# Optimization experiments

Hardware: AMD Instinct MI355X
Metric: run time of the kernel (lower is better)

Reference implementation:

```python
import jax, jax.numpy as jnp
import numpy as np

B, N, P, E = 4096, 1024, 32, 16  # batch, generator dim, n_params, expand_ratio


def setup_inputs() -> dict:
    key = jax.random.key(0)
    k1, k2, k3 = jax.random.split(key, 3)
    x = jax.random.normal(k1, (B, N), dtype=jnp.float32)
    # params ~ stdv*rand - stdv as in the module (stdv=0.01)
    params = 0.01 * jax.random.uniform(k2, (P, E), dtype=jnp.float32) - 0.01
    transformations = jax.random.normal(k3, (P, N, N), dtype=jnp.float32)
    return {"x": x, "params": params, "transformations": transformations}


def reference(x, params, transformations):
    # Fused version of the per-dim loop in ExpandFilterFunctionNew2:
    # filter_e = (params[:, e] @ transformations.flatten(1)).reshape(N, N)
    P_, N_, _ = transformations.shape
    E_ = params.shape[-1]
    filters = jnp.einsum('pe,pq->eq', params, transformations.reshape(P_, -1))
    filters = filters.reshape(E_, N_, N_)              # [E, N, N]
    # output[b, i, e] = sum_j filter[e, i, j] * x[b, j]
    out = jnp.einsum('eij,bj->bie', filters, x)        # [B, N, E]
    # Swish activation (add_linear=False path)
    return out * jax.nn.sigmoid(out)
```

## Files before the change

kernel.cpp:

```cpp
#include <hip/hip_runtime.h>
#include <hip/hip_bf16.h>
#include <stdint.h>

#define BB 4096
#define NN 1024
#define PP 32
#define EE 16
#define NC (NN*EE)

#define BM 256
#define BN 256
#define BK 64
#define NT (NN/BK)

typedef __bf16 bf16x8 __attribute__((ext_vector_type(8)));
typedef float  f32x4  __attribute__((ext_vector_type(4)));

__device__ __forceinline__ void gl2lds16(const void* g, void* l) {
  __builtin_amdgcn_global_load_lds(
      (const __attribute__((address_space(1))) void*)g,
      (__attribute__((address_space(3))) void*)l,
      16, 0, 0);
}

__global__ __launch_bounds__(256) void cvt_x_kernel(
    const float* __restrict__ x, __hip_bfloat16* __restrict__ xb) {
  size_t i4 = (size_t)blockIdx.x * 256 + threadIdx.x;
  float4 v = ((const float4*)x)[i4];
  union { __hip_bfloat16 h[4]; ushort4 u; } pk;
  pk.h[0] = __float2bfloat16(v.x);
  pk.h[1] = __float2bfloat16(v.y);
  pk.h[2] = __float2bfloat16(v.z);
  pk.h[3] = __float2bfloat16(v.w);
  *(ushort4*)(xb + i4 * 4) = pk.u;
}

__global__ __launch_bounds__(256) void make_filters(
    const float* __restrict__ params,
    const float* __restrict__ T,
    __hip_bfloat16* __restrict__ Gt) {
  const int tid = threadIdx.x;
  const int i = blockIdx.x;
  const int j = tid * 4;
  const float4* Tv = (const float4*)T;
  const size_t qv = ((size_t)i * NN + j) >> 2;
  const size_t SLABQ = (size_t)NN * NN / 4;

  float acc[EE][4];
#pragma unroll
  for (int e = 0; e < EE; ++e) {
    acc[e][0] = 0.f; acc[e][1] = 0.f; acc[e][2] = 0.f; acc[e][3] = 0.f;
  }

#pragma unroll 1
  for (int p = 0; p < PP; p += 4) {
    float4 t0 = Tv[(size_t)(p + 0) * SLABQ + qv];
    float4 t1 = Tv[(size_t)(p + 1) * SLABQ + qv];
    float4 t2 = Tv[(size_t)(p + 2) * SLABQ + qv];
    float4 t3 = Tv[(size_t)(p + 3) * SLABQ + qv];
#pragma unroll
    for (int e = 0; e < EE; ++e) {
      float w0 = params[(p + 0) * EE + e];
      float w1 = params[(p + 1) * EE + e];
      float w2 = params[(p + 2) * EE + e];
      float w3 = params[(p + 3) * EE + e];
      acc[e][0] += w0 * t0.x; acc[e][1] += w0 * t0.y;
      acc[e][2] += w0 * t0.z; acc[e][3] += w0 * t0.w;
      acc[e][0] += w1 * t1.x; acc[e][1] += w1 * t1.y;
      acc[e][2] += w1 * t1.z; acc[e][3] += w1 * t1.w;
      acc[e][0] += w2 * t2.x; acc[e][1] += w2 * t2.y;
      acc[e][2] += w2 * t2.z; acc[e][3] += w2 * t2.w;
      acc[e][0] += w3 * t3.x; acc[e][1] += w3 * t3.y;
      acc[e][2] += w3 * t3.z; acc[e][3] += w3 * t3.w;
    }
  }

#pragma unroll
  for (int e = 0; e < EE; ++e) {
    union { __hip_bfloat16 h[4]; ushort4 u; } pk;
    pk.h[0] = __float2bfloat16(acc[e][0]);
    pk.h[1] = __float2bfloat16(acc[e][1]);
    pk.h[2] = __float2bfloat16(acc[e][2]);
    pk.h[3] = __float2bfloat16(acc[e][3]);
    *(ushort4*)&Gt[((size_t)i * EE + e) * NN + j] = pk.u;
  }
}

__global__ __launch_bounds__(512, 2) void gemm_swish(
    const __hip_bfloat16* __restrict__ A,
    const __hip_bfloat16* __restrict__ Bt,
    float* __restrict__ C) {
  __shared__ __hip_bfloat16 lds[2][2][BM * BK];

  const int tid  = threadIdx.x;
  const int wv   = tid >> 6;
  const int lane = tid & 63;
  const int bn   = blockIdx.x;
  const int bm   = blockIdx.y;

  const int srow = wv * 8 + (lane >> 3);
  const int scol = ((lane & 7) ^ (lane >> 3)) * 8;
  const __hip_bfloat16* aSrc = A  + ((size_t)bm * BM + srow) * NN + scol;
  const __hip_bfloat16* bSrc = Bt + ((size_t)bn * BN + srow) * NN + scol;

  const int wm   = (wv >> 2) * 128;
  const int wn   = (wv & 3) * 64;
  const int lrow = lane & 15;
  const int g    = lane >> 4;
  const int xr   = lane & 7;

  f32x4 acc[8][4] = {};

  auto stage = [&](int n_) {
    const int s_  = n_ & 1;
    const int k0_ = n_ * BK;
    char* la = (char*)&lds[s_][0][0] + wv * 1024;
    char* lb = (char*)&lds[s_][1][0] + wv * 1024;
#pragma unroll
    for (int i = 0; i < 4; ++i) {
      gl2lds16(aSrc + (size_t)i * 64 * NN + k0_, la + i * 8192);
      gl2lds16(bSrc + (size_t)i * 64 * NN + k0_, lb + i * 8192);
    }
  };

  stage(0);
  __syncthreads();

  for (int n = 0; n < NT; ++n) {
    if (n + 1 < NT) stage(n + 1);

    const int s = n & 1;
#pragma unroll
    for (int kk = 0; kk < 2; ++kk) {
      bf16x8 af[8], bf[4];
#pragma unroll
      for (int mt = 0; mt < 8; ++mt) {
        const int row = wm + mt * 16 + lrow;
        const int ch  = (kk * 4 + g) ^ xr;
        af[mt] = *(const bf16x8*)&lds[s][0][row * 64 + ch * 8];
      }
#pragma unroll
      for (int nt = 0; nt < 4; ++nt) {
        const int row = wn + nt * 16 + lrow;
        const int ch  = (kk * 4 + g) ^ xr;
        bf[nt] = *(const bf16x8*)&lds[s][1][row * 64 + ch * 8];
      }
#pragma unroll
      for (int mt = 0; mt < 8; ++mt)
#pragma unroll
        for (int nt = 0; nt < 4; ++nt)
          acc[mt][nt] = __builtin_amdgcn_mfma_f32_16x16x32_bf16(
              af[mt], bf[nt], acc[mt][nt], 0, 0, 0);
    }

    __syncthreads();
  }

  const size_t row0 = (size_t)bm * BM + wm + (lane >> 4) * 4;
  const size_t col0 = (size_t)bn * BN + wn + (lane & 15);
#pragma unroll
  for (int mt = 0; mt < 8; ++mt) {
#pragma unroll
    for (int nt = 0; nt < 4; ++nt) {
      const size_t col = col0 + nt * 16;
#pragma unroll
      for (int r = 0; r < 4; ++r) {
        float o = acc[mt][nt][r];
        float s = o * __builtin_amdgcn_rcpf(1.0f + __expf(-o));
        C[(row0 + mt * 16 + r) * NC + col] = s;
      }
    }
  }
}

extern "C" void kernel_launch(void* const* d_in, const int* in_sizes, int n_in,
                              void* d_out, int out_size, void* d_ws, size_t ws_size,
                              hipStream_t stream) {
  const float* x      = (const float*)d_in[0];
  const float* params = (const float*)d_in[1];
  const float* T      = (const float*)d_in[2];
  float* out = (float*)d_out;

  __hip_bfloat16* Gt = (__hip_bfloat16*)d_ws;
  __hip_bfloat16* xb = (__hip_bfloat16*)((char*)d_ws + (size_t)NC * NN * 2);

  cvt_x_kernel<<<(BB * NN / 4) / 256, 256, 0, stream>>>(x, xb);
  make_filters<<<NN, 256, 0, stream>>>(params, T, Gt);
  gemm_swish<<<dim3(NC / BN, BB / BM), 512, 0, stream>>>(xb, Gt, out);
}
```

Baseline: 471.5 us.

## Split GEMM prefetch across k-halves, add barrier and MFMA priority boost

```diff
diff --git a/kernel.cpp b/kernel.cpp
--- a/kernel.cpp
+++ b/kernel.cpp
@@ -53,25 +53,19 @@
   }
 
 #pragma unroll 1
-  for (int p = 0; p < PP; p += 4) {
-    float4 t0 = Tv[(size_t)(p + 0) * SLABQ + qv];
-    float4 t1 = Tv[(size_t)(p + 1) * SLABQ + qv];
-    float4 t2 = Tv[(size_t)(p + 2) * SLABQ + qv];
-    float4 t3 = Tv[(size_t)(p + 3) * SLABQ + qv];
+  for (int p0 = 0; p0 < PP; p0 += 8) {
+    float4 t[8];
 #pragma unroll
-    for (int e = 0; e < EE; ++e) {
-      float w0 = params[(p + 0) * EE + e];
-      float w1 = params[(p + 1) * EE + e];
-      float w2 = params[(p + 2) * EE + e];
-      float w3 = params[(p + 3) * EE + e];
-      acc[e][0] += w0 * t0.x; acc[e][1] += w0 * t0.y;
-      acc[e][2] += w0 * t0.z; acc[e][3] += w0 * t0.w;
-      acc[e][0] += w1 * t1.x; acc[e][1] += w1 * t1.y;
-      acc[e][2] += w1 * t1.z; acc[e][3] += w1 * t1.w;
-      acc[e][0] += w2 * t2.x; acc[e][1] += w2 * t2.y;
-      acc[e][2] += w2 * t2.z; acc[e][3] += w2 * t2.w;
-      acc[e][0] += w3 * t3.x; acc[e][1] += w3 * t3.y;
-      acc[e][2] += w3 * t3.z; acc[e][3] += w3 * t3.w;
+    for (int u = 0; u < 8; ++u)
+      t[u] = Tv[(size_t)(p0 + u) * SLABQ + qv];
+#pragma unroll
+    for (int u = 0; u < 8; ++u) {
+#pragma unroll
+      for (int e = 0; e < EE; ++e) {
+        float w = params[(p0 + u) * EE + e];
+        acc[e][0] += w * t[u].x; acc[e][1] += w * t[u].y;
+        acc[e][2] += w * t[u].z; acc[e][3] += w * t[u].w;
+      }
     }
   }
 
@@ -111,46 +105,44 @@
 
   f32x4 acc[8][4] = {};
 
-  auto stage = [&](int n_) {
+  auto stage_half = [&](int n_, int h_) {
     const int s_  = n_ & 1;
     const int k0_ = n_ * BK;
-    char* la = (char*)&lds[s_][0][0] + wv * 1024;
-    char* lb = (char*)&lds[s_][1][0] + wv * 1024;
+    const __hip_bfloat16* src = h_ ? bSrc : aSrc;
+    char* dst = (char*)&lds[s_][h_][0] + wv * 1024;
 #pragma unroll
-    for (int i = 0; i < 4; ++i) {
-      gl2lds16(aSrc + (size_t)i * 64 * NN + k0_, la + i * 8192);
-      gl2lds16(bSrc + (size_t)i * 64 * NN + k0_, lb + i * 8192);
-    }
+    for (int i = 0; i < 4; ++i)
+      gl2lds16(src + (size_t)i * 64 * NN + k0_, dst + i * 8192);
   };
 
-  stage(0);
+  stage_half(0, 0);
+  stage_half(0, 1);
   __syncthreads();
 
   for (int n = 0; n < NT; ++n) {
-    if (n + 1 < NT) stage(n + 1);
-
     const int s = n & 1;
 #pragma unroll
     for (int kk = 0; kk < 2; ++kk) {
+      if (n + 1 < NT) stage_half(n + 1, kk);
+
       bf16x8 af[8], bf[4];
+      const int ch = (kk * 4 + g) ^ xr;
 #pragma unroll
-      for (int mt = 0; mt < 8; ++mt) {
-        const int row = wm + mt * 16 + lrow;
-        const int ch  = (kk * 4 + g) ^ xr;
-        af[mt] = *(const bf16x8*)&lds[s][0][row * 64 + ch * 8];
-      }
+      for (int mt = 0; mt < 8; ++mt)
+        af[mt] = *(const bf16x8*)&lds[s][0][(wm + mt * 16 + lrow) * 64 + ch * 8];
 #pragma unroll
-      for (int nt = 0; nt < 4; ++nt) {
-        const int row = wn + nt * 16 + lrow;
-        const int ch  = (kk * 4 + g) ^ xr;
-        bf[nt] = *(const bf16x8*)&lds[s][1][row * 64 + ch * 8];
-      }
+      for (int nt = 0; nt < 4; ++nt)
+        bf[nt] = *(const bf16x8*)&lds[s][1][(wn + nt * 16 + lrow) * 64 + ch * 8];
+
+      __builtin_amdgcn_s_barrier();
+      __builtin_amdgcn_s_setprio(1);
 #pragma unroll
       for (int mt = 0; mt < 8; ++mt)
 #pragma unroll
         for (int nt = 0; nt < 4; ++nt)
           acc[mt][nt] = __builtin_amdgcn_mfma_f32_16x16x32_bf16(
               af[mt], bf[nt], acc[mt][nt], 0, 0, 0);
+      __builtin_amdgcn_s_setprio(0);
     }
 
     __syncthreads();
```

Measured after the change: 462.5 us. Within noise of the previous version (-1.9%).
